# Optimization experiments

Measured on AMD Instinct MI355X. Metric: run time of the kernel, lower is better.

Reference implementation:

```python
import jax, jax.numpy as jnp
import numpy as np

B, CIN, H, W = 8, 512, 32, 32
NH = 8
DQ = DK = DV = 256  # int(0.5 * Cin)
COUT = 512


def setup_inputs() -> dict:
    key = jax.random.key(0)
    k0, k1, k2, k3, k4 = jax.random.split(key, 5)
    x = jax.random.normal(k0, (B, CIN, H, W), dtype=jnp.float32)
    # 1x1 conv weights stored as [out, in] matrices (kernel size 1)
    w_qkv = jax.random.normal(k1, (DQ + DK + DV, CIN), dtype=jnp.float32) * 0.02
    b_qkv = jax.random.normal(k2, (DQ + DK + DV,), dtype=jnp.float32) * 0.02
    w_attn = jax.random.normal(k3, (COUT, DV), dtype=jnp.float32) * 0.02
    b_attn = jax.random.normal(k4, (COUT,), dtype=jnp.float32) * 0.02
    return {"x": x, "w_qkv": w_qkv, "b_qkv": b_qkv, "w_attn": w_attn, "b_attn": b_attn}


def _split_heads(t):
    b, c, h, w = t.shape
    return t.reshape(b, NH, c // NH, h, w)


def reference(x, w_qkv, b_qkv, w_attn, b_attn):
    b, _, h, w = x.shape
    hw = h * w
    # 1x1 conv == per-pixel GEMM
    qkv = jnp.einsum('bchw,oc->bohw', x, w_qkv) + b_qkv[None, :, None, None]
    q = qkv[:, :DQ]
    k = qkv[:, DQ:DQ + DK]
    v = qkv[:, DQ + DK:]
    dkh = DK // NH
    q = _split_heads(q) * (dkh ** -0.5)
    k = _split_heads(k)
    v = _split_heads(v)
    flat_q = q.reshape(b, NH, DQ // NH, hw)
    flat_k = k.reshape(b, NH, DK // NH, hw)
    flat_v = v.reshape(b, NH, DV // NH, hw)
    # logits: [b, NH, hw, hw]  (q^T k over feature dim)
    logits = jnp.einsum('bndq,bndk->bnqk', flat_q, flat_k)
    # FAITHFUL quirk: softmax over the HEAD axis (dim=1), as in the source
    weights = jax.nn.softmax(logits, axis=1)
    # attn_out: [b, NH, hw, dvh]
    attn_out = jnp.einsum('bnqk,bndk->bnqd', weights, flat_v)
    # FAITHFUL quirk: raw reshape (no transpose) to [b, NH, dvh, H, W]
    attn_out = attn_out.reshape(b, NH, DV // NH, h, w).reshape(b, DV, h, w)
    out = jnp.einsum('bchw,oc->bohw', attn_out, w_attn) + b_attn[None, :, None, None]
    return out
```

## Files before the change

kernel.cpp:

```cpp
#include <hip/hip_runtime.h>
#include <math.h>

#define BATCH 8
#define CIN   512
#define DQKV  768
#define NHEAD 8
#define HW    1024

typedef __attribute__((ext_vector_type(8))) short  short8;
typedef __attribute__((ext_vector_type(4))) float  float4v;

__device__ __forceinline__ ushort f2bf(float f) {
    union { float f; unsigned u; } c; c.f = f;
    unsigned u = c.u + 0x7fffu + ((c.u >> 16) & 1u);
    return (ushort)(u >> 16);
}

__device__ __forceinline__ void async_ld16(const ushort* g, ushort* l) {
    auto gp = (const __attribute__((address_space(1))) unsigned int*)g;
    auto lp = (__attribute__((address_space(3))) unsigned int*)l;
    __builtin_amdgcn_global_load_lds(gp, lp, 16, 0, 0);
}

__global__ __launch_bounds__(256)
void transpose_cvt(const float* __restrict__ in, ushort* __restrict__ out,
                   int K, int N)
{
    __shared__ float Ts[64][65];
    const int b  = blockIdx.z;
    const int k0 = blockIdx.y * 64;
    const int n0 = blockIdx.x * 64;
    const int t  = threadIdx.x;
    const float* ib = in + (size_t)b * K * N;
    ushort*      ob = out + (size_t)b * N * K;

    const int r  = t >> 4;
    const int c4 = (t & 15) * 4;
    #pragma unroll
    for (int p = 0; p < 4; ++p) {
        float4 v = *(const float4*)(ib + (size_t)(k0 + r + 16 * p) * N + n0 + c4);
        Ts[r + 16 * p][c4 + 0] = v.x;
        Ts[r + 16 * p][c4 + 1] = v.y;
        Ts[r + 16 * p][c4 + 2] = v.z;
        Ts[r + 16 * p][c4 + 3] = v.w;
    }
    __syncthreads();

    const int nl = t >> 3;
    const int kc = (t & 7) * 8;
    #pragma unroll
    for (int p = 0; p < 2; ++p) {
        int n = nl + 32 * p;
        uint4 u;
        u.x = (uint)f2bf(Ts[kc + 0][n]) | ((uint)f2bf(Ts[kc + 1][n]) << 16);
        u.y = (uint)f2bf(Ts[kc + 2][n]) | ((uint)f2bf(Ts[kc + 3][n]) << 16);
        u.z = (uint)f2bf(Ts[kc + 4][n]) | ((uint)f2bf(Ts[kc + 5][n]) << 16);
        u.w = (uint)f2bf(Ts[kc + 6][n]) | ((uint)f2bf(Ts[kc + 7][n]) << 16);
        *(uint4*)(ob + (size_t)(n0 + n) * K + k0 + kc) = u;
    }
}

__global__ void cvt_bf16(const float* __restrict__ in, ushort* __restrict__ out, int n8)
{
    int i = blockIdx.x * blockDim.x + threadIdx.x;
    if (i >= n8) return;
    const float4* p = (const float4*)(in + (size_t)i * 8);
    float4 a = p[0], b = p[1];
    uint4 u;
    u.x = (uint)f2bf(a.x) | ((uint)f2bf(a.y) << 16);
    u.y = (uint)f2bf(a.z) | ((uint)f2bf(a.w) << 16);
    u.z = (uint)f2bf(b.x) | ((uint)f2bf(b.y) << 16);
    u.w = (uint)f2bf(b.z) | ((uint)f2bf(b.w) << 16);
    *(uint4*)(out + (size_t)i * 8) = u;
}

template<int M, int K, bool QSCALE, bool OUTBF>
__global__ __launch_bounds__(256, 2)
void gemm_bt(const ushort* __restrict__ A, const ushort* __restrict__ Bt,
             const float* __restrict__ bias, void* __restrict__ Oo)
{
    __shared__ __align__(16) ushort As[128 * 64];
    __shared__ __align__(16) ushort Bs[128 * 64];

    const int b    = blockIdx.z;
    const int m0   = blockIdx.y * 128;
    const int n0   = blockIdx.x * 128;
    const int t    = threadIdx.x;
    const int lane = t & 63;
    const int wave = t >> 6;
    const int l16  = lane & 15;
    const int quad = lane >> 4;
    const int wm   = (wave & 1) * 64;
    const int wn   = (wave >> 1) * 64;

    const ushort* Bb = Bt + (size_t)b * HW * K;

    float4v acc[4][4];
    #pragma unroll
    for (int i = 0; i < 4; ++i)
        #pragma unroll
        for (int j = 0; j < 4; ++j)
            acc[i][j] = (float4v){0.f, 0.f, 0.f, 0.f};

    const int srow = t >> 3;
    const int sg   = t & 7;

    for (int k0 = 0; k0 < K; k0 += 64) {
        __syncthreads();
        #pragma unroll
        for (int is = 0; is < 4; ++is) {
            int row = srow + is * 32;
            int gch = sg ^ (row & 7);
            async_ld16(A  + (size_t)(m0 + row) * K + k0 + gch * 8,
                       As + (size_t)t * 8 + is * 2048);
            async_ld16(Bb + (size_t)(n0 + row) * K + k0 + gch * 8,
                       Bs + (size_t)t * 8 + is * 2048);
        }
        __syncthreads();

        #pragma unroll
        for (int ks = 0; ks < 2; ++ks) {
            short8 af[4], bf[4];
            #pragma unroll
            for (int i = 0; i < 4; ++i) {
                int row = wm + i * 16 + l16;
                int ch  = (ks * 4 + quad) ^ (row & 7);
                af[i] = *(const short8*)&As[row * 64 + ch * 8];
            }
            #pragma unroll
            for (int j = 0; j < 4; ++j) {
                int row = wn + j * 16 + l16;
                int ch  = (ks * 4 + quad) ^ (row & 7);
                bf[j] = *(const short8*)&Bs[row * 64 + ch * 8];
            }
            #pragma unroll
            for (int i = 0; i < 4; ++i)
                #pragma unroll
                for (int j = 0; j < 4; ++j)
                    acc[i][j] = __builtin_amdgcn_mfma_f32_16x16x32_bf16(
                        af[i], bf[j], acc[i][j], 0, 0, 0);
        }
    }

    #pragma unroll
    for (int i = 0; i < 4; ++i) {
        #pragma unroll
        for (int rr = 0; rr < 4; ++rr) {
            int m = m0 + wm + i * 16 + quad * 4 + rr;
            float bi = bias[m];
            float sc = QSCALE ? ((m < 256) ? 0.17677669529663687f : 1.0f) : 1.0f;
            #pragma unroll
            for (int j = 0; j < 4; ++j) {
                int n = n0 + wn + j * 16 + l16;
                float val = (acc[i][j][rr] + bi) * sc;
                if (OUTBF)
                    ((ushort*)Oo)[((size_t)b * M + m) * HW + n] = f2bf(val);
                else
                    ((float*)Oo)[((size_t)b * M + m) * HW + n] = val;
            }
        }
    }
}

__global__ __launch_bounds__(256, 2)
void attn_kernel(const ushort* __restrict__ qkv, float* __restrict__ attn)
{
    __shared__ __align__(16) ushort Qs[NHEAD * 16 * 40];
    __shared__ __align__(16) ushort Ks[NHEAD * 32 * 40];
    __shared__ __align__(16) ushort Vs[NHEAD * 32 * 40];
    __shared__ __align__(16) ushort Ws[NHEAD * 16 * 40];
    __shared__ float  Ss[NHEAD * 529];

    const int t    = threadIdx.x;
    const int b    = blockIdx.y;
    const int q0   = blockIdx.x * 16;
    const int wave = t >> 6;
    const int lane = t & 63;
    const int l16  = lane & 15;
    const int quad = lane >> 4;

    const ushort* qk = qkv + (size_t)b * DQKV * HW;

    #pragma unroll
    for (int p = 0; p < 2; ++p) {
        int tt  = t + p * 256;
        int row = tt >> 1;
        int c8  = (tt & 1) * 8;
        uint4 u = *(const uint4*)(qk + (size_t)row * HW + q0 + c8);
        ushort v[8]; *(uint4*)v = u;
        int n = row >> 5, d = row & 31;
        ushort* dst = &Qs[(n * 16 + c8) * 40 + d];
        #pragma unroll
        for (int j = 0; j < 8; ++j) dst[j * 40] = v[j];
    }

    float4v acc[2][2];
    #pragma unroll
    for (int i = 0; i < 2; ++i)
        #pragma unroll
        for (int j = 0; j < 2; ++j)
            acc[i][j] = (float4v){0.f, 0.f, 0.f, 0.f};

    const int sq = t >> 4;
    const int sk = (t & 15) * 2;

    for (int k0 = 0; k0 < HW; k0 += 32) {
        __syncthreads();

        #pragma unroll
        for (int p = 0; p < 4; ++p) {
            int tt  = t + p * 256;
            int row = tt >> 2;
            int c8  = (tt & 3) * 8;
            int n = row >> 5, d = row & 31;
            uint4 ku = *(const uint4*)(qk + (size_t)(256 + row) * HW + k0 + c8);
            ushort kv[8]; *(uint4*)kv = ku;
            ushort* dK = &Ks[(n * 32 + c8) * 40 + d];
            #pragma unroll
            for (int j = 0; j < 8; ++j) dK[j * 40] = kv[j];
            uint4 vu = *(const uint4*)(qk + (size_t)(512 + row) * HW + k0 + c8);
            *(uint4*)&Vs[(n * 32 + d) * 40 + c8] = vu;
        }
        __syncthreads();

        #pragma unroll
        for (int hh = 0; hh < 2; ++hh) {
            int h = wave * 2 + hh;
            short8 a = *(const short8*)&Qs[(h * 16 + l16) * 40 + quad * 8];
            #pragma unroll
            for (int ko = 0; ko < 2; ++ko) {
                short8 bfr = *(const short8*)&Ks[(h * 32 + ko * 16 + l16) * 40 + quad * 8];
                float4v s = __builtin_amdgcn_mfma_f32_16x16x32_bf16(
                    a, bfr, (float4v){0.f, 0.f, 0.f, 0.f}, 0, 0, 0);
                float* sp = &Ss[h * 529 + (quad * 4) * 33 + ko * 16 + l16];
                #pragma unroll
                for (int r = 0; r < 4; ++r) sp[r * 33] = s[r];
            }
        }
        __syncthreads();

        {
            float v[NHEAD][2];
            float m0v = -1e30f, m1v = -1e30f;
            #pragma unroll
            for (int n = 0; n < NHEAD; ++n) {
                v[n][0] = Ss[n * 529 + sq * 33 + sk + 0];
                v[n][1] = Ss[n * 529 + sq * 33 + sk + 1];
                m0v = fmaxf(m0v, v[n][0]);
                m1v = fmaxf(m1v, v[n][1]);
            }
            float s0 = 0.f, s1 = 0.f;
            #pragma unroll
            for (int n = 0; n < NHEAD; ++n) {
                v[n][0] = __expf(v[n][0] - m0v);
                v[n][1] = __expf(v[n][1] - m1v);
                s0 += v[n][0];
                s1 += v[n][1];
            }
            float i0 = 1.0f / s0, i1 = 1.0f / s1;
            #pragma unroll
            for (int n = 0; n < NHEAD; ++n) {
                uint pk = (uint)f2bf(v[n][0] * i0) | ((uint)f2bf(v[n][1] * i1) << 16);
                *(uint*)&Ws[(n * 16 + sq) * 40 + sk] = pk;
            }
        }
        __syncthreads();

        #pragma unroll
        for (int hh = 0; hh < 2; ++hh) {
            int h = wave * 2 + hh;
            short8 a = *(const short8*)&Ws[(h * 16 + l16) * 40 + quad * 8];
            #pragma unroll
            for (int dd = 0; dd < 2; ++dd) {
                short8 bfr = *(const short8*)&Vs[(h * 32 + dd * 16 + l16) * 40 + quad * 8];
                acc[hh][dd] = __builtin_amdgcn_mfma_f32_16x16x32_bf16(
                    a, bfr, acc[hh][dd], 0, 0, 0);
            }
        }
    }

    #pragma unroll
    for (int hh = 0; hh < 2; ++hh) {
        int h = wave * 2 + hh;
        #pragma unroll
        for (int dd = 0; dd < 2; ++dd) {
            #pragma unroll
            for (int r = 0; r < 4; ++r) {
                int qg = q0 + quad * 4 + r;
                size_t addr = ((size_t)b * 256 + h * 32 + (qg >> 5)) * HW
                            + (size_t)(qg & 31) * 32 + dd * 16 + l16;
                attn[addr] = acc[hh][dd][r];
            }
        }
    }
}

extern "C" void kernel_launch(void* const* d_in, const int* in_sizes, int n_in,
                              void* d_out, int out_size, void* d_ws, size_t ws_size,
                              hipStream_t stream)
{
    const float* x      = (const float*)d_in[0];
    const float* w_qkv  = (const float*)d_in[1];
    const float* b_qkv  = (const float*)d_in[2];
    const float* w_attn = (const float*)d_in[3];
    const float* b_attn = (const float*)d_in[4];
    float* out = (float*)d_out;

    ushort* qkv_b   = (ushort*)d_ws;
    float*  attn_ws = (float*)((char*)d_ws + 12582912);
    ushort* xb      = (ushort*)((char*)d_ws + 12582912 + 8388608);
    ushort* ab      = xb;
    ushort* wb1     = xb + 4194304;
    ushort* wb2     = wb1 + 393216;

    cvt_bf16<<<192, 256, 0, stream>>>(w_qkv, wb1, 49152);
    cvt_bf16<<<64, 256, 0, stream>>>(w_attn, wb2, 16384);
    transpose_cvt<<<dim3(16, 8, BATCH), 256, 0, stream>>>(x, xb, CIN, HW);

    gemm_bt<DQKV, CIN, true, true>
        <<<dim3(8, 6, BATCH), 256, 0, stream>>>(wb1, xb, b_qkv, qkv_b);

    attn_kernel<<<dim3(HW / 16, BATCH), 256, 0, stream>>>(qkv_b, attn_ws);

    transpose_cvt<<<dim3(16, 4, BATCH), 256, 0, stream>>>(attn_ws, ab, 256, HW);

    gemm_bt<512, 256, false, false>
        <<<dim3(8, 4, BATCH), 256, 0, stream>>>(wb2, ab, b_attn, out);
}
```

Measured before the change: 185.1 us.

## Pre-transpose Q/K once and write attention output directly as bf16 transposed

Adds a qk_transform kernel that rewrites Q and K into a [b, head, hw, 32] layout, so the attention kernel loads them with vector stores into LDS instead of scalar transposing scatter stores. Previously every one of the 64 query blocks per batch re-transposed all of K. The attention kernel now writes its output directly in bf16, in the transposed layout the second GEMM expects, which removes the fp32 workspace and the separate transpose_cvt launch. The cost is an extra kernel launch and extra global traffic for the Qt/Kt copies, and the final output stores are strided 2-byte scatters.

```diff
diff --git a/kernel.cpp b/kernel.cpp
--- a/kernel.cpp
+++ b/kernel.cpp
@@ -74,6 +74,38 @@
     *(uint4*)(out + (size_t)i * 8) = u;
 }
 
+__global__ __launch_bounds__(256)
+void qk_transform(const ushort* __restrict__ qkv, ushort* __restrict__ Qt,
+                  ushort* __restrict__ Kt)
+{
+    __shared__ ushort Ts[32 * 264];
+    const int b   = blockIdx.z;
+    const int g   = blockIdx.y;
+    const int sp0 = blockIdx.x * 256;
+    const int t   = threadIdx.x;
+
+    const ushort* src = qkv + ((size_t)b * DQKV + g * 32) * HW;
+    ushort* dst = (g < 8 ? Qt : Kt) + ((size_t)b * NHEAD + (g & 7)) * (HW * 32);
+
+    #pragma unroll
+    for (int p = 0; p < 4; ++p) {
+        int d = (t >> 5) + p * 8;
+        int c = t & 31;
+        uint4 u = *(const uint4*)(src + (size_t)d * HW + sp0 + c * 8);
+        *(uint4*)&Ts[d * 264 + c * 8] = u;
+    }
+    __syncthreads();
+
+    ushort* orow = dst + (size_t)(sp0 + t) * 32;
+    #pragma unroll
+    for (int c = 0; c < 4; ++c) {
+        ushort v[8];
+        #pragma unroll
+        for (int j = 0; j < 8; ++j) v[j] = Ts[(c * 8 + j) * 264 + t];
+        *(uint4*)(orow + c * 8) = *(uint4*)v;
+    }
+}
+
 template<int M, int K, bool QSCALE, bool OUTBF>
 __global__ __launch_bounds__(256, 2)
 void gemm_bt(const ushort* __restrict__ A, const ushort* __restrict__ Bt,
@@ -163,7 +195,8 @@
 }
 
 __global__ __launch_bounds__(256, 2)
-void attn_kernel(const ushort* __restrict__ qkv, float* __restrict__ attn)
+void attn_kernel(const ushort* __restrict__ qkv, const ushort* __restrict__ Qt,
+                 const ushort* __restrict__ Kt, ushort* __restrict__ ab)
 {
     __shared__ __align__(16) ushort Qs[NHEAD * 16 * 40];
     __shared__ __align__(16) ushort Ks[NHEAD * 32 * 40];
@@ -179,19 +212,16 @@
     const int l16  = lane & 15;
     const int quad = lane >> 4;
 
-    const ushort* qk = qkv + (size_t)b * DQKV * HW;
+    const ushort* qk  = qkv + (size_t)b * DQKV * HW;
+    const ushort* Qtb = Qt + (size_t)b * NHEAD * HW * 32;
+    const ushort* Ktb = Kt + (size_t)b * NHEAD * HW * 32;
 
     #pragma unroll
     for (int p = 0; p < 2; ++p) {
-        int tt  = t + p * 256;
-        int row = tt >> 1;
-        int c8  = (tt & 1) * 8;
-        uint4 u = *(const uint4*)(qk + (size_t)row * HW + q0 + c8);
-        ushort v[8]; *(uint4*)v = u;
-        int n = row >> 5, d = row & 31;
-        ushort* dst = &Qs[(n * 16 + c8) * 40 + d];
-        #pragma unroll
-        for (int j = 0; j < 8; ++j) dst[j * 40] = v[j];
+        int idx = t + p * 256;
+        int n = idx >> 6, q = (idx >> 2) & 15, c = idx & 3;
+        uint4 u = *(const uint4*)(Qtb + (size_t)n * (HW * 32) + (size_t)(q0 + q) * 32 + c * 8);
+        *(uint4*)&Qs[(n * 16 + q) * 40 + c * 8] = u;
     }
 
     float4v acc[2][2];
@@ -209,17 +239,12 @@
 
         #pragma unroll
         for (int p = 0; p < 4; ++p) {
-            int tt  = t + p * 256;
-            int row = tt >> 2;
-            int c8  = (tt & 3) * 8;
-            int n = row >> 5, d = row & 31;
-            uint4 ku = *(const uint4*)(qk + (size_t)(256 + row) * HW + k0 + c8);
-            ushort kv[8]; *(uint4*)kv = ku;
-            ushort* dK = &Ks[(n * 32 + c8) * 40 + d];
-            #pragma unroll
-            for (int j = 0; j < 8; ++j) dK[j * 40] = kv[j];
-            uint4 vu = *(const uint4*)(qk + (size_t)(512 + row) * HW + k0 + c8);
-            *(uint4*)&Vs[(n * 32 + d) * 40 + c8] = vu;
+            int idx = t + p * 256;
+            int n = idx >> 7, r = (idx >> 2) & 31, c = idx & 3;
+            uint4 ku = *(const uint4*)(Ktb + (size_t)n * (HW * 32) + (size_t)(k0 + r) * 32 + c * 8);
+            *(uint4*)&Ks[(n * 32 + r) * 40 + c * 8] = ku;
+            uint4 vu = *(const uint4*)(qk + (size_t)(512 + n * 32 + r) * HW + k0 + c * 8);
+            *(uint4*)&Vs[(n * 32 + r) * 40 + c * 8] = vu;
         }
         __syncthreads();
 
@@ -284,12 +309,13 @@
         int h = wave * 2 + hh;
         #pragma unroll
         for (int dd = 0; dd < 2; ++dd) {
+            int d = dd * 16 + l16;
             #pragma unroll
             for (int r = 0; r < 4; ++r) {
                 int qg = q0 + quad * 4 + r;
-                size_t addr = ((size_t)b * 256 + h * 32 + (qg >> 5)) * HW
-                            + (size_t)(qg & 31) * 32 + dd * 16 + l16;
-                attn[addr] = acc[hh][dd][r];
+                size_t addr = ((size_t)b * HW + (size_t)((qg & 31) * 32 + d)) * 256
+                            + h * 32 + (qg >> 5);
+                ab[addr] = f2bf(acc[hh][dd][r]);
             }
         }
     }
@@ -306,12 +332,13 @@
     const float* b_attn = (const float*)d_in[4];
     float* out = (float*)d_out;
 
-    ushort* qkv_b   = (ushort*)d_ws;
-    float*  attn_ws = (float*)((char*)d_ws + 12582912);
-    ushort* xb      = (ushort*)((char*)d_ws + 12582912 + 8388608);
-    ushort* ab      = xb;
-    ushort* wb1     = xb + 4194304;
-    ushort* wb2     = wb1 + 393216;
+    ushort* qkv_b = (ushort*)d_ws;
+    ushort* xb    = qkv_b + 6291456;
+    ushort* Qt    = xb;
+    ushort* Kt    = xb + 2097152;
+    ushort* ab    = xb + 4194304;
+    ushort* wb1   = ab + 2097152;
+    ushort* wb2   = wb1 + 393216;
 
     cvt_bf16<<<192, 256, 0, stream>>>(w_qkv, wb1, 49152);
     cvt_bf16<<<64, 256, 0, stream>>>(w_attn, wb2, 16384);
@@ -320,9 +347,9 @@
     gemm_bt<DQKV, CIN, true, true>
         <<<dim3(8, 6, BATCH), 256, 0, stream>>>(wb1, xb, b_qkv, qkv_b);
 
-    attn_kernel<<<dim3(HW / 16, BATCH), 256, 0, stream>>>(qkv_b, attn_ws);
-
-    transpose_cvt<<<dim3(16, 4, BATCH), 256, 0, stream>>>(attn_ws, ab, 256, HW);
+    qk_transform<<<dim3(4, 16, BATCH), 256, 0, stream>>>(qkv_b, Qt, Kt);
+
+    attn_kernel<<<dim3(HW / 16, BATCH), 256, 0, stream>>>(qkv_b, Qt, Kt, ab);
 
     gemm_bt<512, 256, false, false>
         <<<dim3(8, 4, BATCH), 256, 0, stream>>>(wb2, ab, b_attn, out);
```

Result: faster. 178.2 us (-3.7%).
